# Performance work log

Measured on AMD Instinct MI355X. Metric: run time of the kernel, lower is better.

Reference implementation:

```python
import jax, jax.numpy as jnp
import numpy as np

D_MODEL = 512

def setup_inputs() -> dict:
    key = jax.random.key(0)
    k1, k2, k3, k4, k5 = jax.random.split(key, 5)
    x = jax.random.normal(k1, (8, D_MODEL, 2048), dtype=jnp.float32)
    s = 1.0 / np.sqrt(D_MODEL)
    W_qkv = jax.random.uniform(k2, (D_MODEL, 3 * D_MODEL), dtype=jnp.float32, minval=-s, maxval=s)
    b_qkv = jax.random.uniform(k3, (3 * D_MODEL,), dtype=jnp.float32, minval=-s, maxval=s)
    W_proj = jax.random.uniform(k4, (D_MODEL, D_MODEL), dtype=jnp.float32, minval=-s, maxval=s)
    b_proj = jax.random.uniform(k5, (D_MODEL,), dtype=jnp.float32, minval=-s, maxval=s)
    return {"x": x, "W_qkv": W_qkv, "b_qkv": b_qkv, "W_proj": W_proj, "b_proj": b_proj}

def reference(x, W_qkv, b_qkv, W_proj, b_proj):
    # x: [B, L, N] with L == d_model; attend across the N variable axis
    xt = jnp.swapaxes(x, 1, 2)                      # [B, N, L]
    L = xt.shape[-1]
    qkv = xt @ W_qkv + b_qkv                        # [B, N, 3L]
    q, k, v = jnp.split(qkv, 3, axis=-1)            # each [B, N, L]
    attn = jnp.einsum('bnd,bmd->bnm', q, k) / jnp.sqrt(jnp.float32(L))
    attn = jax.nn.softmax(attn, axis=-1)            # [B, N, N]
    out = jnp.einsum('bnm,bmd->bnd', attn, v)       # [B, N, L]
    out = out @ W_proj + b_proj                     # [B, N, L]
    return jnp.swapaxes(out, 1, 2)                  # [B, L, N]
```

## Files before the change

kernel.cpp:

```cpp
#include <hip/hip_runtime.h>

#define NVAR 2048
#define DM   512
#define J3   1536

typedef _Float16 f16;
typedef _Float16 f16x8 __attribute__((ext_vector_type(8)));
typedef _Float16 f16x4 __attribute__((ext_vector_type(4)));
typedef float    f32x4 __attribute__((ext_vector_type(4)));

#define SBAR() do { asm volatile("s_barrier" ::: "memory"); \
                    __builtin_amdgcn_sched_barrier(0); } while(0)
#define LGKM0() do { asm volatile("s_waitcnt lgkmcnt(0)" ::: "memory"); \
                     __builtin_amdgcn_sched_barrier(0); } while(0)
#define GLOAD(gp, lp) __builtin_amdgcn_global_load_lds( \
    (const __attribute__((address_space(1))) void*)(gp), \
    (__attribute__((address_space(3))) void*)(lp), 16, 0, 0)

__device__ __forceinline__ void waitvm_n(int n) {
    switch (n) {
    case 0: asm volatile("s_waitcnt vmcnt(0)" ::: "memory"); break;
    case 1: asm volatile("s_waitcnt vmcnt(1)" ::: "memory"); break;
    case 2: asm volatile("s_waitcnt vmcnt(2)" ::: "memory"); break;
    case 3: asm volatile("s_waitcnt vmcnt(3)" ::: "memory"); break;
    case 4: asm volatile("s_waitcnt vmcnt(4)" ::: "memory"); break;
    case 5: asm volatile("s_waitcnt vmcnt(5)" ::: "memory"); break;
    case 6: asm volatile("s_waitcnt vmcnt(6)" ::: "memory"); break;
    case 7: asm volatile("s_waitcnt vmcnt(7)" ::: "memory"); break;
    case 8: asm volatile("s_waitcnt vmcnt(8)" ::: "memory"); break;
    default: break;
    }
    __builtin_amdgcn_sched_barrier(0);
}

__global__ __launch_bounds__(256)
void k_tr(const float* __restrict__ src, f16* __restrict__ dst,
          int R, int C, long bsSrc, long bsDst) {
    __shared__ float t[64][65];
    const float* s = src + (size_t)blockIdx.z * bsSrc;
    f16* d = dst + (size_t)blockIdx.z * bsDst;
    const int c0 = blockIdx.x * 64, r0 = blockIdx.y * 64;
    const int lx = threadIdx.x & 15, ly = threadIdx.x >> 4;
#pragma unroll
    for (int p = 0; p < 4; ++p) {
        int r = p * 16 + ly;
        f32x4 v = *(const f32x4*)(s + (size_t)(r0 + r) * C + c0 + lx * 4);
#pragma unroll
        for (int i = 0; i < 4; ++i) t[r][lx * 4 + i] = v[i];
    }
    __syncthreads();
#pragma unroll
    for (int p = 0; p < 4; ++p) {
        int c = p * 16 + ly;
        f16x4 h;
#pragma unroll
        for (int i = 0; i < 4; ++i) h[i] = (f16)t[lx * 4 + i][c];
        *(f16x4*)(d + (size_t)(c0 + c) * R + r0 + lx * 4) = h;
    }
}

__global__ __launch_bounds__(256)
void k_prep(const float* __restrict__ Wqkv, const float* __restrict__ Wproj,
            const float* __restrict__ bqkv,
            f16* __restrict__ WqT, f16* __restrict__ WpT,
            f16* __restrict__ Wq2, float* __restrict__ bias_c) {
    __shared__ float t[64][65];
    const int b = blockIdx.x;
    if (b < 192) {
        const float* s; f16* d; int R, C, bx, by;
        if (b < 128) { s = Wqkv; d = WqT; R = DM; C = J3; bx = b & 15; by = b >> 4; }
        else { s = Wproj; d = WpT; R = DM; C = DM; bx = (b - 128) & 7; by = (b - 128) >> 3; }
        const int c0 = bx * 64, r0 = by * 64;
        const int lx = threadIdx.x & 15, ly = threadIdx.x >> 4;
#pragma unroll
        for (int p = 0; p < 4; ++p) {
            int r = p * 16 + ly;
            f32x4 v = *(const f32x4*)(s + (size_t)(r0 + r) * C + c0 + lx * 4);
#pragma unroll
            for (int i = 0; i < 4; ++i) t[r][lx * 4 + i] = v[i];
        }
        __syncthreads();
#pragma unroll
        for (int p = 0; p < 4; ++p) {
            int c = p * 16 + ly;
            f16x4 h;
#pragma unroll
            for (int i = 0; i < 4; ++i) h[i] = (f16)t[lx * 4 + i][c];
            *(f16x4*)(d + (size_t)(c0 + c) * R + r0 + lx * 4) = h;
        }
    } else if (b < 448) {
        int idx = (b - 192) * 256 + threadIdx.x;
        int gi = idx * 4;
        int d = gi >> 9, j = gi & 511;
        f32x4 v = *(const f32x4*)(Wqkv + (size_t)d * J3 + 1024 + j);
        f16x4 h;
#pragma unroll
        for (int i = 0; i < 4; ++i) h[i] = (f16)v[i];
        *(f16x4*)(Wq2 + (size_t)d * 512 + j) = h;
    } else {
        const int bb = b - 448;
        const int lt = threadIdx.x & 63, js = threadIdx.x >> 6;
        const int l = bb * 64 + lt;
        float s = 0.f;
        for (int j = js * 128; j < js * 128 + 128; ++j)
            s += bqkv[1024 + j] * Wproj[(size_t)j * DM + l];
        float* red = &t[0][0];
        red[js * 64 + lt] = s;
        __syncthreads();
        if (js == 0)
            bias_c[1024 + l] = (red[lt] + red[64 + lt]) + (red[128 + lt] + red[192 + lt]);
        if (threadIdx.x < 128) {
            int i = bb * 128 + threadIdx.x;
            bias_c[i] = bqkv[i];
        }
    }
}

#define ASZ (256 * 64)
template<int MODE, int ABITS>
__global__ __launch_bounds__(512, 2)
void gemm_sp(const f16* __restrict__ A, const f16* __restrict__ B,
             long bsA, long bsB, int lda, int ldb, int K,
             const float* __restrict__ bias, float scale,
             f16* __restrict__ o0, f16* __restrict__ o1) {
    __shared__ f16 smem[5 * ASZ];
    f16* sA = smem;
    f16* sB = smem + 3 * ASZ;

    const int tid  = threadIdx.x;
    const int lane = tid & 63;
    const int w    = __builtin_amdgcn_readfirstlane(tid >> 6);
    const int wm   = (w >> 2) * 128;
    const int wn   = (w & 3) * 64;
    const int z    = blockIdx.x;
    const int bid  = blockIdx.y;
    const int bxA  = bid & ((1 << ABITS) - 1);
    const int bxB  = bid >> ABITS;

    const f16* Ab = A + (size_t)z * bsA + (size_t)bxA * 256 * lda;
    const f16* Bb = B + (size_t)z * bsB + (size_t)bxB * 256 * ldb;

    int offA[2][2], offB[2][2];
#pragma unroll
    for (int h = 0; h < 2; ++h)
#pragma unroll
        for (int i = 0; i < 2; ++i) {
            int slot = i * 512 + tid;
            int row  = h * 128 + (slot >> 3);
            int s    = (slot & 7) ^ (row & 7);
            offA[h][i] = row * lda + s * 8;
            offB[h][i] = row * ldb + s * 8;
        }

    auto STG_A = [&](int kt, int h, int buf) {
        f16* d = sA + buf * ASZ + h * 8192;
#pragma unroll
        for (int i = 0; i < 2; ++i)
            GLOAD(Ab + offA[h][i] + kt * 64, d + (i * 512 + tid) * 8);
    };
    auto STG_B = [&](int kt, int h, int buf) {
        f16* d = sB + buf * ASZ + h * 8192;
#pragma unroll
        for (int i = 0; i < 2; ++i)
            GLOAD(Bb + offB[h][i] + kt * 64, d + (i * 512 + tid) * 8);
    };

    int koff[2];
#pragma unroll
    for (int ks = 0; ks < 2; ++ks)
        koff[ks] = ((ks * 4 + (lane >> 4)) ^ (lane & 7)) * 8;
    const int rowA = (wm + (lane & 15)) * 64;
    const int rowB = (wn + (lane & 15)) * 64;

    f16x8 av[8][2], bv[4][2];
    f32x4 acc[8][4] = {};

    auto LD_AV = [&](const f16* p, int mi0) {
#pragma unroll
        for (int mi = 0; mi < 4; ++mi)
#pragma unroll
            for (int ks = 0; ks < 2; ++ks)
                av[mi0 + mi][ks] = *(const f16x8*)(p + rowA + (mi0 + mi) * 1024 + koff[ks]);
    };
    auto LD_BV = [&](const f16* p, int nj0) {
#pragma unroll
        for (int nj = 0; nj < 2; ++nj)
#pragma unroll
            for (int ks = 0; ks < 2; ++ks)
                bv[nj0 + nj][ks] = *(const f16x8*)(p + rowB + (nj0 + nj) * 1024 + koff[ks]);
    };
    auto MM = [&](int mi0, int nj0) {
        __builtin_amdgcn_s_setprio(1);
#pragma unroll
        for (int mi = 0; mi < 4; ++mi)
#pragma unroll
            for (int nj = 0; nj < 2; ++nj)
#pragma unroll
                for (int ks = 0; ks < 2; ++ks)
                    acc[mi0 + mi][nj0 + nj] = __builtin_amdgcn_mfma_f32_16x16x32_f16(
                        av[mi0 + mi][ks], bv[nj0 + nj][ks], acc[mi0 + mi][nj0 + nj], 0, 0, 0);
        __builtin_amdgcn_s_setprio(0);
    };

    const int NT = K >> 6;
    int issued = 0, markB = 0;

    STG_A(0, 0, 0); STG_A(0, 1, 0); issued += 4;
    STG_B(0, 0, 0); STG_B(0, 1, 0); issued += 4; markB = issued;
    if (NT > 1) { STG_A(1, 0, 1); STG_A(1, 1, 1); issued += 4; }
    waitvm_n(issued - markB);
    SBAR();

    int iA = 0, iB = 0;
    for (int t = 0; t < NT; ++t) {
        const f16* pA = sA + iA * ASZ;
        const f16* pB = sB + iB * ASZ;
        const int bufB2 = iB ^ 1;
        int bufA2 = iA + 2; if (bufA2 >= 3) bufA2 -= 3;

        LD_BV(pB, 0); LD_AV(pA, 0);
        if (t + 1 < NT) { STG_B(t + 1, 0, bufB2); issued += 2; }
        SBAR(); LGKM0();
        MM(0, 0);
        SBAR();

        LD_BV(pB, 2);
        if (t + 1 < NT) { STG_B(t + 1, 1, bufB2); issued += 2; markB = issued; }
        SBAR(); LGKM0();
        MM(0, 2);
        SBAR();

        LD_AV(pA, 4);
        if (t + 2 < NT) { STG_A(t + 2, 0, bufA2); issued += 2; }
        SBAR(); LGKM0();
        MM(4, 2);
        SBAR();

        if (t + 2 < NT) { STG_A(t + 2, 1, bufA2); issued += 2; }
        if (t + 1 < NT) { waitvm_n(issued - markB); SBAR(); }
        MM(4, 0);
        if (t + 1 < NT) SBAR();

        iA = (iA + 1 == 3) ? 0 : iA + 1;
        iB ^= 1;
    }

    if (MODE == 0) {
        const int seg = bxA >> 1;
        f16* dst = seg ? o1 : o0;
        const int rb0 = bxA * 256 + wm + (lane >> 4) * 4;
        const int cb0 = bxB * 256 + wn + (lane & 15);
#pragma unroll
        for (int mi = 0; mi < 8; ++mi) {
            const int j = rb0 + mi * 16;
            const int jj = j - seg * 512;
            const f32x4 b4 = *(const f32x4*)(bias + j);
#pragma unroll
            for (int nj = 0; nj < 4; ++nj) {
                const int n = cb0 + nj * 16;
                f16x4 vv;
#pragma unroll
                for (int r = 0; r < 4; ++r) vv[r] = (f16)(acc[mi][nj][r] + b4[r]);
                *(f16x4*)(dst + ((size_t)z * NVAR + n) * DM + jj) = vv;
            }
        }
    } else {
        const int n0 = bxB * 256;
        const int m0 = bxA * 256;
        f16* bb = smem;
#pragma unroll
        for (int mi = 0; mi < 8; ++mi) {
            const int m    = wm + mi * 16 + ((lane >> 4) << 2);
            const int c16  = m >> 3;
            const int half = m & 4;
#pragma unroll
            for (int nj = 0; nj < 4; ++nj) {
                const int nl = wn + nj * 16 + (lane & 15);
                f16x4 vv;
#pragma unroll
                for (int r = 0; r < 4; ++r)
                    vv[r] = (f16)__expf(acc[mi][nj][r] * scale);
                *(f16x4*)(bb + nl * 256 + ((c16 ^ (nl & 7)) << 3) + half) = vv;
            }
        }
        LGKM0();
        SBAR();
#pragma unroll
        for (int it = 0; it < 16; ++it) {
            const int row = it * 16 + (tid >> 5);
            const int ch  = tid & 31;
            f16x8 v = *(const f16x8*)(bb + row * 256 + ((ch ^ (row & 7)) << 3));
            *(f16x8*)(o0 + ((size_t)z * NVAR + n0 + row) * NVAR + m0 + ch * 8) = v;
        }
    }
}

#define AO (128 * 64)
#define BO (256 * 64)
__global__ __launch_bounds__(512, 2)
void gemm_out(const f16* __restrict__ A, const f16* __restrict__ B,
              long bsA, long bsB, int lda, int ldb, int K,
              const float* __restrict__ bias, float* __restrict__ of) {
    __shared__ f16 smem[3 * AO + 2 * BO];
    f16* sA = smem;
    f16* sB = smem + 3 * AO;

    const int tid  = threadIdx.x;
    const int lane = tid & 63;
    const int w    = __builtin_amdgcn_readfirstlane(tid >> 6);
    const int wm   = (w >> 2) * 64;
    const int wn   = (w & 3) * 64;
    const int z    = blockIdx.x;
    const int bid  = blockIdx.y;
    const int bxA  = bid & 15;
    const int bxB  = bid >> 4;

    const f16* Ab = A + (size_t)z * bsA + (size_t)bxA * 128 * lda;
    const f16* Bb = B + (size_t)z * bsB + (size_t)bxB * 256 * ldb;

    int offA[2], offB[4];
#pragma unroll
    for (int i = 0; i < 2; ++i) {
        int slot = i * 512 + tid;
        int row  = slot >> 3;
        int s    = (slot & 7) ^ (row & 7);
        offA[i] = row * lda + s * 8;
    }
#pragma unroll
    for (int i = 0; i < 4; ++i) {
        int slot = i * 512 + tid;
        int row  = slot >> 3;
        int s    = (slot & 7) ^ (row & 7);
        offB[i] = row * ldb + s * 8;
    }

    auto STG_A = [&](int kt, int buf) {
        f16* d = sA + buf * AO;
#pragma unroll
        for (int i = 0; i < 2; ++i)
            GLOAD(Ab + offA[i] + kt * 64, d + (i * 512 + tid) * 8);
    };
    auto STG_B = [&](int kt, int buf) {
        f16* d = sB + buf * BO;
#pragma unroll
        for (int i = 0; i < 4; ++i)
            GLOAD(Bb + offB[i] + kt * 64, d + (i * 512 + tid) * 8);
    };

    int koff[2];
#pragma unroll
    for (int ks = 0; ks < 2; ++ks)
        koff[ks] = ((ks * 4 + (lane >> 4)) ^ (lane & 7)) * 8;
    const int rowA = (wm + (lane & 15)) * 64;
    const int rowB = (wn + (lane & 15)) * 64;

    f16x8 ones;
#pragma unroll
    for (int e = 0; e < 8; ++e) ones[e] = (f16)1.0f;

    f16x8 av[4][2], bv[4][2];
    f32x4 acc[4][4] = {};
    f32x4 accrs[4] = {};

    auto LD_AV = [&](const f16* p, int mi0) {
#pragma unroll
        for (int mi = 0; mi < 2; ++mi)
#pragma unroll
            for (int ks = 0; ks < 2; ++ks)
                av[mi0 + mi][ks] = *(const f16x8*)(p + rowA + (mi0 + mi) * 1024 + koff[ks]);
    };
    auto LD_BV = [&](const f16* p) {
#pragma unroll
        for (int nj = 0; nj < 4; ++nj)
#pragma unroll
            for (int ks = 0; ks < 2; ++ks)
                bv[nj][ks] = *(const f16x8*)(p + rowB + nj * 1024 + koff[ks]);
    };
    auto MM = [&](int mi0) {
        __builtin_amdgcn_s_setprio(1);
#pragma unroll
        for (int mi = 0; mi < 2; ++mi)
#pragma unroll
            for (int ks = 0; ks < 2; ++ks) {
                accrs[mi0 + mi] = __builtin_amdgcn_mfma_f32_16x16x32_f16(
                    av[mi0 + mi][ks], ones, accrs[mi0 + mi], 0, 0, 0);
#pragma unroll
                for (int nj = 0; nj < 4; ++nj)
                    acc[mi0 + mi][nj] = __builtin_amdgcn_mfma_f32_16x16x32_f16(
                        av[mi0 + mi][ks], bv[nj][ks], acc[mi0 + mi][nj], 0, 0, 0);
            }
        __builtin_amdgcn_s_setprio(0);
    };

    const int NT = K >> 6;
    int issued = 0, markB = 0;

    STG_A(0, 0); issued += 2;
    STG_B(0, 0); issued += 4; markB = issued;
    if (NT > 1) { STG_A(1, 1); issued += 2; }
    waitvm_n(issued - markB);
    SBAR();

    int iA = 0, iB = 0;
    for (int t = 0; t < NT; ++t) {
        const f16* pA = sA + iA * AO;
        const f16* pB = sB + iB * BO;
        int bufA2 = iA + 2; if (bufA2 >= 3) bufA2 -= 3;

        LD_BV(pB); LD_AV(pA, 0);
        if (t + 1 < NT) { STG_B(t + 1, iB ^ 1); issued += 4; markB = issued; }
        SBAR(); LGKM0();
        MM(0);
        SBAR();

        LD_AV(pA, 2);
        if (t + 2 < NT) { STG_A(t + 2, bufA2); issued += 2; }
        SBAR(); LGKM0();
        MM(2);
        if (t + 1 < NT) { waitvm_n(issued - markB); SBAR(); }

        iA = (iA + 1 == 3) ? 0 : iA + 1;
        iB ^= 1;
    }

    const int rb0 = bxA * 128 + wm + (lane >> 4) * 4;
    const int cb0 = bxB * 256 + wn + (lane & 15);
#pragma unroll
    for (int mi = 0; mi < 4; ++mi) {
        f32x4 inv;
#pragma unroll
        for (int r = 0; r < 4; ++r) inv[r] = 1.0f / accrs[mi][r];
#pragma unroll
        for (int nj = 0; nj < 4; ++nj) {
            const int l = cb0 + nj * 16;
            const float bb = bias[l];
            f32x4 vv;
#pragma unroll
            for (int r = 0; r < 4; ++r) vv[r] = acc[mi][nj][r] * inv[r] + bb;
            *(f32x4*)(of + ((size_t)z * DM + l) * NVAR + rb0 + mi * 16) = vv;
        }
    }
}

template<int MODE>
__global__ __launch_bounds__(256)
void gemm_f16(const f16* __restrict__ A, const f16* __restrict__ B,
              long bsA, long bsB, int lda, int ldb, int K, int nbx,
              const float* __restrict__ bias, f16* __restrict__ o0) {
    __shared__ f16 sA[128 * 64];
    __shared__ f16 sB[128 * 64];
    const int tid  = threadIdx.x;
    const int lane = tid & 63;
    const int w    = __builtin_amdgcn_readfirstlane(tid >> 6);
    const int wm   = (w >> 1) * 64;
    const int wn   = (w & 1) * 64;
    const int z    = blockIdx.x;
    const int bid  = blockIdx.y;
    const int bxA  = bid % nbx;
    const int bxB  = bid / nbx;

    const f16* Ab = A + (size_t)z * bsA + (size_t)bxA * 128 * lda;
    const f16* Bb = B + (size_t)z * bsB + (size_t)bxB * 128 * ldb;

    int srcA[4], srcB[4];
#pragma unroll
    for (int i = 0; i < 4; ++i) {
        int slot = i * 256 + tid;
        int row  = slot >> 3;
        int s    = (slot & 7) ^ (row & 7);
        srcA[i] = row * lda + s * 8;
        srcB[i] = row * ldb + s * 8;
    }

    f32x4 acc[4][4] = {};

    for (int k0 = 0; k0 < K; k0 += 64) {
        __syncthreads();
#pragma unroll
        for (int i = 0; i < 4; ++i) {
            GLOAD(Ab + srcA[i] + k0, sA + i * 2048 + w * 512);
            GLOAD(Bb + srcB[i] + k0, sB + i * 2048 + w * 512);
        }
        __syncthreads();
#pragma unroll
        for (int kh = 0; kh < 2; ++kh) {
            f16x8 av[4], bv[4];
#pragma unroll
            for (int mi = 0; mi < 4; ++mi) {
                int r = wm + mi * 16 + (lane & 15);
                int s = (kh * 4 + (lane >> 4)) ^ (r & 7);
                av[mi] = *(const f16x8*)(sA + r * 64 + s * 8);
            }
#pragma unroll
            for (int nj = 0; nj < 4; ++nj) {
                int r = wn + nj * 16 + (lane & 15);
                int s = (kh * 4 + (lane >> 4)) ^ (r & 7);
                bv[nj] = *(const f16x8*)(sB + r * 64 + s * 8);
            }
#pragma unroll
            for (int mi = 0; mi < 4; ++mi)
#pragma unroll
                for (int nj = 0; nj < 4; ++nj)
                    acc[mi][nj] = __builtin_amdgcn_mfma_f32_16x16x32_f16(
                        av[mi], bv[nj], acc[mi][nj], 0, 0, 0);
        }
    }

    const int rb0 = bxA * 128 + wm + (lane >> 4) * 4;
    const int cb0 = bxB * 128 + wn + (lane & 15);

    if (MODE == 4) {
#pragma unroll
        for (int mi = 0; mi < 4; ++mi)
#pragma unroll
            for (int nj = 0; nj < 4; ++nj) {
                f16x4 vv;
#pragma unroll
                for (int r = 0; r < 4; ++r) vv[r] = (f16)acc[mi][nj][r];
                *(f16x4*)(o0 + ((size_t)(cb0 + nj * 16)) * DM
                               + rb0 + mi * 16) = vv;
            }
    } else {
#pragma unroll
        for (int mi = 0; mi < 4; ++mi)
#pragma unroll
            for (int nj = 0; nj < 4; ++nj) {
                const int l = cb0 + nj * 16;
                const float bb = bias[l];
                f16x4 vv;
#pragma unroll
                for (int r = 0; r < 4; ++r) vv[r] = (f16)(acc[mi][nj][r] + bb);
                *(f16x4*)(o0 + ((size_t)z * DM + l) * NVAR + rb0 + mi * 16) = vv;
            }
    }
}

extern "C" void kernel_launch(void* const* d_in, const int* in_sizes, int n_in,
                              void* d_out, int out_size, void* d_ws, size_t ws_size,
                              hipStream_t stream) {
    const float* x     = (const float*)d_in[0];
    const float* Wqkv  = (const float*)d_in[1];
    const float* bqkv  = (const float*)d_in[2];
    const float* Wproj = (const float*)d_in[3];
    const float* bproj = (const float*)d_in[4];
    float* out = (float*)d_out;

    const size_t PB = (size_t)NVAR * DM;
    f16* xT   = (f16*)d_ws;
    f16* q    = xT + 8 * PB;
    f16* kk   = q  + 8 * PB;
    f16* vwT  = kk + 8 * PB;
    f16* S    = vwT + 8 * PB;
    f16* scr  = S  + (size_t)8 * NVAR * NVAR;
    f16* WqT  = scr + 8 * PB;
    f16* WvpT = WqT + (size_t)1024 * DM;
    f16* WpT  = WqT + (size_t)J3 * DM;
    f16* Wq2  = scr;
    float* bias_c = (float*)(scr + 512 * 512);

    k_tr<<<dim3(NVAR / 64, DM / 64, 8), 256, 0, stream>>>(
        x, xT, DM, NVAR, (long)DM * NVAR, (long)NVAR * DM);
    k_prep<<<dim3(456), 256, 0, stream>>>(Wqkv, Wproj, bqkv, WqT, WpT, Wq2, bias_c);

    gemm_f16<4><<<dim3(1, 16), 256, 0, stream>>>(
        Wq2, WpT, 0, 0, 512, DM, DM, 4, nullptr, WvpT);

    gemm_sp<0, 2><<<dim3(8, 4 * 8), 512, 0, stream>>>(
        WqT, xT, 0, (long)NVAR * DM, DM, DM, DM,
        bias_c, 1.f, q, kk);

    gemm_f16<5><<<dim3(8, 16 * 4), 256, 0, stream>>>(
        xT, WvpT, (long)NVAR * DM, 0, DM, DM, DM, 16,
        bias_c + 1024, vwT);

    gemm_sp<1, 3><<<dim3(8, 8 * 8), 512, 0, stream>>>(
        kk, q, (long)NVAR * DM, (long)NVAR * DM, DM, DM, DM,
        nullptr, 0.044194173824159216f, S, nullptr);

    gemm_out<<<dim3(8, 32), 512, 0, stream>>>(
        S, vwT, (long)NVAR * NVAR, (long)DM * NVAR, NVAR, NVAR, NVAR,
        bproj, out);
}
```

Before: 178.2 us.

## Fuse Q, K and V projections into a single gemm_f16 launch

The Q/K projection, previously run by the pipelined 256-tile gemm_sp, and the separate V-times-Wproj projection are merged into one gemm_f16 launch. It covers all 1536 output rows (12 row blocks of 128) against xT and routes each block's epilogue to q, kk or the transposed vwT buffer. gemm_sp is reduced to the QK^T/exp path only. This removes one launch and lets the three projections share scheduling, but the Q/K part now runs on the simpler 128-tile, non-pipelined GEMM. The V segment also writes the transposed output with scalar, partially coalesced stores.

```diff
diff --git a/kernel.cpp b/kernel.cpp
--- a/kernel.cpp
+++ b/kernel.cpp
@@ -117,12 +117,10 @@
 }
 
 #define ASZ (256 * 64)
-template<int MODE, int ABITS>
 __global__ __launch_bounds__(512, 2)
 void gemm_sp(const f16* __restrict__ A, const f16* __restrict__ B,
              long bsA, long bsB, int lda, int ldb, int K,
-             const float* __restrict__ bias, float scale,
-             f16* __restrict__ o0, f16* __restrict__ o1) {
+             float scale, f16* __restrict__ o0) {
     __shared__ f16 smem[5 * ASZ];
     f16* sA = smem;
     f16* sB = smem + 3 * ASZ;
@@ -134,8 +132,8 @@
     const int wn   = (w & 3) * 64;
     const int z    = blockIdx.x;
     const int bid  = blockIdx.y;
-    const int bxA  = bid & ((1 << ABITS) - 1);
-    const int bxB  = bid >> ABITS;
+    const int bxA  = bid & 7;
+    const int bxB  = bid >> 3;
 
     const f16* Ab = A + (size_t)z * bsA + (size_t)bxA * 256 * lda;
     const f16* Bb = B + (size_t)z * bsB + (size_t)bxB * 256 * ldb;
@@ -245,53 +243,32 @@
         iB ^= 1;
     }
 
-    if (MODE == 0) {
-        const int seg = bxA >> 1;
-        f16* dst = seg ? o1 : o0;
-        const int rb0 = bxA * 256 + wm + (lane >> 4) * 4;
-        const int cb0 = bxB * 256 + wn + (lane & 15);
-#pragma unroll
-        for (int mi = 0; mi < 8; ++mi) {
-            const int j = rb0 + mi * 16;
-            const int jj = j - seg * 512;
-            const f32x4 b4 = *(const f32x4*)(bias + j);
-#pragma unroll
-            for (int nj = 0; nj < 4; ++nj) {
-                const int n = cb0 + nj * 16;
-                f16x4 vv;
-#pragma unroll
-                for (int r = 0; r < 4; ++r) vv[r] = (f16)(acc[mi][nj][r] + b4[r]);
-                *(f16x4*)(dst + ((size_t)z * NVAR + n) * DM + jj) = vv;
-            }
-        }
-    } else {
-        const int n0 = bxB * 256;
-        const int m0 = bxA * 256;
-        f16* bb = smem;
-#pragma unroll
-        for (int mi = 0; mi < 8; ++mi) {
-            const int m    = wm + mi * 16 + ((lane >> 4) << 2);
-            const int c16  = m >> 3;
-            const int half = m & 4;
-#pragma unroll
-            for (int nj = 0; nj < 4; ++nj) {
-                const int nl = wn + nj * 16 + (lane & 15);
-                f16x4 vv;
-#pragma unroll
-                for (int r = 0; r < 4; ++r)
-                    vv[r] = (f16)__expf(acc[mi][nj][r] * scale);
-                *(f16x4*)(bb + nl * 256 + ((c16 ^ (nl & 7)) << 3) + half) = vv;
-            }
-        }
-        LGKM0();
-        SBAR();
-#pragma unroll
-        for (int it = 0; it < 16; ++it) {
-            const int row = it * 16 + (tid >> 5);
-            const int ch  = tid & 31;
-            f16x8 v = *(const f16x8*)(bb + row * 256 + ((ch ^ (row & 7)) << 3));
-            *(f16x8*)(o0 + ((size_t)z * NVAR + n0 + row) * NVAR + m0 + ch * 8) = v;
-        }
+    const int n0 = bxB * 256;
+    const int m0 = bxA * 256;
+    f16* bb = smem;
+#pragma unroll
+    for (int mi = 0; mi < 8; ++mi) {
+        const int m    = wm + mi * 16 + ((lane >> 4) << 2);
+        const int c16  = m >> 3;
+        const int half = m & 4;
+#pragma unroll
+        for (int nj = 0; nj < 4; ++nj) {
+            const int nl = wn + nj * 16 + (lane & 15);
+            f16x4 vv;
+#pragma unroll
+            for (int r = 0; r < 4; ++r)
+                vv[r] = (f16)__expf(acc[mi][nj][r] * scale);
+            *(f16x4*)(bb + nl * 256 + ((c16 ^ (nl & 7)) << 3) + half) = vv;
+        }
+    }
+    LGKM0();
+    SBAR();
+#pragma unroll
+    for (int it = 0; it < 16; ++it) {
+        const int row = it * 16 + (tid >> 5);
+        const int ch  = tid & 31;
+        f16x8 v = *(const f16x8*)(bb + row * 256 + ((ch ^ (row & 7)) << 3));
+        *(f16x8*)(o0 + ((size_t)z * NVAR + n0 + row) * NVAR + m0 + ch * 8) = v;
     }
 }
 
@@ -446,7 +423,8 @@
 __global__ __launch_bounds__(256)
 void gemm_f16(const f16* __restrict__ A, const f16* __restrict__ B,
               long bsA, long bsB, int lda, int ldb, int K, int nbx,
-              const float* __restrict__ bias, f16* __restrict__ o0) {
+              const float* __restrict__ bias,
+              f16* __restrict__ o0, f16* __restrict__ o1, f16* __restrict__ o2) {
     __shared__ f16 sA[128 * 64];
     __shared__ f16 sB[128 * 64];
     const int tid  = threadIdx.x;
@@ -509,7 +487,31 @@
     const int rb0 = bxA * 128 + wm + (lane >> 4) * 4;
     const int cb0 = bxB * 128 + wn + (lane & 15);
 
-    if (MODE == 4) {
+    if (MODE == 0) {
+        const int seg = (bxA * 128) >> 9;
+#pragma unroll
+        for (int mi = 0; mi < 4; ++mi) {
+            const int j = rb0 + mi * 16;
+            const f32x4 b4 = *(const f32x4*)(bias + j);
+#pragma unroll
+            for (int nj = 0; nj < 4; ++nj) {
+                const int n = cb0 + nj * 16;
+                if (seg == 2) {
+#pragma unroll
+                    for (int r = 0; r < 4; ++r)
+                        o2[((size_t)z * DM + (j - 1024 + r)) * NVAR + n] =
+                            (f16)(acc[mi][nj][r] + b4[r]);
+                } else {
+                    f16* dst = seg ? o1 : o0;
+                    const int jj = seg ? j - 512 : j;
+                    f16x4 vv;
+#pragma unroll
+                    for (int r = 0; r < 4; ++r) vv[r] = (f16)(acc[mi][nj][r] + b4[r]);
+                    *(f16x4*)(dst + ((size_t)z * NVAR + n) * DM + jj) = vv;
+                }
+            }
+        }
+    } else {
 #pragma unroll
         for (int mi = 0; mi < 4; ++mi)
 #pragma unroll
@@ -519,18 +521,6 @@
                 for (int r = 0; r < 4; ++r) vv[r] = (f16)acc[mi][nj][r];
                 *(f16x4*)(o0 + ((size_t)(cb0 + nj * 16)) * DM
                                + rb0 + mi * 16) = vv;
-            }
-    } else {
-#pragma unroll
-        for (int mi = 0; mi < 4; ++mi)
-#pragma unroll
-            for (int nj = 0; nj < 4; ++nj) {
-                const int l = cb0 + nj * 16;
-                const float bb = bias[l];
-                f16x4 vv;
-#pragma unroll
-                for (int r = 0; r < 4; ++r) vv[r] = (f16)(acc[mi][nj][r] + bb);
-                *(f16x4*)(o0 + ((size_t)z * DM + l) * NVAR + rb0 + mi * 16) = vv;
             }
     }
 }
@@ -563,19 +553,15 @@
     k_prep<<<dim3(456), 256, 0, stream>>>(Wqkv, Wproj, bqkv, WqT, WpT, Wq2, bias_c);
 
     gemm_f16<4><<<dim3(1, 16), 256, 0, stream>>>(
-        Wq2, WpT, 0, 0, 512, DM, DM, 4, nullptr, WvpT);
-
-    gemm_sp<0, 2><<<dim3(8, 4 * 8), 512, 0, stream>>>(
-        WqT, xT, 0, (long)NVAR * DM, DM, DM, DM,
-        bias_c, 1.f, q, kk);
-
-    gemm_f16<5><<<dim3(8, 16 * 4), 256, 0, stream>>>(
-        xT, WvpT, (long)NVAR * DM, 0, DM, DM, DM, 16,
-        bias_c + 1024, vwT);
-
-    gemm_sp<1, 3><<<dim3(8, 8 * 8), 512, 0, stream>>>(
+        Wq2, WpT, 0, 0, 512, DM, DM, 4, nullptr, WvpT, nullptr, nullptr);
+
+    gemm_f16<0><<<dim3(8, 12 * 16), 256, 0, stream>>>(
+        WqT, xT, 0, (long)NVAR * DM, DM, DM, DM, 12,
+        bias_c, q, kk, vwT);
+
+    gemm_sp<<<dim3(8, 8 * 8), 512, 0, stream>>>(
         kk, q, (long)NVAR * DM, (long)NVAR * DM, DM, DM, DM,
-        nullptr, 0.044194173824159216f, S, nullptr);
+        0.044194173824159216f, S);
 
     gemm_out<<<dim3(8, 32), 512, 0, stream>>>(
         S, vwT, (long)NVAR * NVAR, (long)DM * NVAR, NVAR, NVAR, NVAR,
```

New measurement: 178.1 us. No clear change (-0.0%).
